# Kernel optimization log

Hardware: AMD Instinct MI355X
Metric: run time of the kernel (lower is better)

## Reference

```python
import jax, jax.numpy as jnp
import numpy as np

N_MET = 100_000
N_RXN = 50_000
E_SUB = 2_000_000
E_ALL = 4_000_000
MSG_DIM = 16
HIDDEN = 32


def setup_inputs() -> dict:
    key = jax.random.key(0)
    ks = jax.random.split(key, 16)
    x_met = jax.random.normal(ks[0], (N_MET,), dtype=jnp.float32)
    sto_sub = jax.random.uniform(ks[1], (E_SUB,), dtype=jnp.float32, minval=0.0, maxval=1.0)
    sto_all = jax.random.normal(ks[2], (E_ALL,), dtype=jnp.float32)
    met_sub = jax.random.randint(ks[3], (E_SUB,), 0, N_MET)
    rxn_sub = jax.random.randint(ks[4], (E_SUB,), 0, N_RXN)
    met_all = jax.random.randint(ks[5], (E_ALL,), 0, N_MET)
    rxn_all = jax.random.randint(ks[6], (E_ALL,), 0, N_RXN)
    # msg_mlp: Linear(2->HIDDEN), Tanh, Linear(HIDDEN->MSG_DIM)
    W1m = jax.random.normal(ks[7], (2, HIDDEN), jnp.float32) / np.sqrt(2.0)
    b1m = jnp.zeros((HIDDEN,), jnp.float32)
    W2m = jax.random.normal(ks[8], (HIDDEN, MSG_DIM), jnp.float32) / np.sqrt(HIDDEN)
    b2m = jnp.zeros((MSG_DIM,), jnp.float32)
    # rate_mlp: Linear(MSG_DIM->HIDDEN), Tanh, Linear(HIDDEN->1)
    W1r = jax.random.normal(ks[9], (MSG_DIM, HIDDEN), jnp.float32) / np.sqrt(MSG_DIM)
    b1r = jnp.zeros((HIDDEN,), jnp.float32)
    W2r = jax.random.normal(ks[10], (HIDDEN, 1), jnp.float32) / np.sqrt(HIDDEN)
    b2r = jnp.zeros((1,), jnp.float32)
    return {
        "x_met": x_met, "sto_sub": sto_sub, "sto_all": sto_all,
        "W1m": W1m, "b1m": b1m, "W2m": W2m, "b2m": b2m,
        "W1r": W1r, "b1r": b1r, "W2r": W2r, "b2r": b2r,
        "met_sub": met_sub, "rxn_sub": rxn_sub,
        "met_all": met_all, "rxn_all": rxn_all,
    }


def reference(x_met, sto_sub, sto_all, W1m, b1m, W2m, b2m, W1r, b1r, W2r, b2r,
              met_sub, rxn_sub, met_all, rxn_all):
    # gather substrate node features and build per-edge MLP input [E_sub, 2]
    msg_in = jnp.stack([x_met[met_sub], sto_sub], axis=-1)
    # msg MLP: tanh hidden, linear out -> [E_sub, MSG_DIM]
    msg = jnp.tanh(msg_in @ W1m + b1m) @ W2m + b2m
    # scatter-add messages into reactions -> [N_RXN, MSG_DIM]
    h_rxn = jax.ops.segment_sum(msg, rxn_sub, num_segments=N_RXN)
    # rate MLP + softplus -> per-reaction rate v [N_RXN]
    v = jax.nn.softplus((jnp.tanh(h_rxn @ W1r + b1r) @ W2r + b2r)[:, 0])
    # stoichiometric contributions scattered into metabolites -> dxdt [N_MET]
    contrib = sto_all * v[rxn_all]
    dxdt = jax.ops.segment_sum(contrib, met_all, num_segments=N_MET)
    return dxdt, v
```

## Files before the change

### kernel.cpp

```cpp
#include <hip/hip_runtime.h>

#define N_MET 100000
#define N_RXN 50000
#define E_SUB 2000000
#define E_ALL 4000000
#define MSG_DIM 16
#define HIDDEN 32

#define NBKT_A 391
#define NB_ALL 245
#define TILE_A 16384
#define LOFFA_W (NBKT_A + 1)
#define NBKT_S 782
#define NB_SUB 245
#define TILE_S 8192
#define SLOT_S 4096


__device__ __forceinline__ float fast_tanh(float x) {
    const float e = __expf(2.0f * x);
    return 1.0f - 2.0f * __builtin_amdgcn_rcpf(e + 1.0f);
}

__global__ __launch_bounds__(1024) void zero_gcnt_kernel(int* __restrict__ g)
{
    const int t = threadIdx.x;
    if (t < NBKT_S) g[t] = 0;
}


__global__ __launch_bounds__(1024) void scatter_bin_sub_kernel(
    const float* __restrict__ x_met, const float* __restrict__ sto_sub,
    const int* __restrict__ met_sub, const int* __restrict__ rxn_sub,
    int* __restrict__ gcnt, float2* __restrict__ pxs)
{
    __shared__ float2 se[TILE_S];
    __shared__ int cnt[NBKT_S];
    __shared__ int loff[NBKT_S + 1];
    __shared__ int roff[NBKT_S];
    const int t = threadIdx.x, bk = blockIdx.x;
    for (int i = t; i < NBKT_S; i += 1024) cnt[i] = 0;
    __syncthreads();

    const int e0 = bk * TILE_S;
    const int rem = min(TILE_S, E_SUB - e0);
    const int tb = 8 * t;
    float2 pay[8]; int meta[8];
    if (tb + 8 <= rem) {
        const int4 r01 = ((const int4*)(rxn_sub + e0))[2 * t];
        const int4 r23 = ((const int4*)(rxn_sub + e0))[2 * t + 1];
        const int4 m01 = ((const int4*)(met_sub + e0))[2 * t];
        const int4 m23 = ((const int4*)(met_sub + e0))[2 * t + 1];
        const float4 s01 = ((const float4*)(sto_sub + e0))[2 * t];
        const float4 s23 = ((const float4*)(sto_sub + e0))[2 * t + 1];
        const int rr[8] = {r01.x, r01.y, r01.z, r01.w, r23.x, r23.y, r23.z, r23.w};
        const int mm[8] = {m01.x, m01.y, m01.z, m01.w, m23.x, m23.y, m23.z, m23.w};
        const float ss[8] = {s01.x, s01.y, s01.z, s01.w, s23.x, s23.y, s23.z, s23.w};
#pragma unroll
        for (int k = 0; k < 8; ++k) {
            const int r = rr[k];
            const float x = x_met[mm[k]];
            const int sb = (__float_as_int(ss[k]) & ~63) | (r & 63);
            pay[k] = make_float2(x, __int_as_float(sb));
            const int q = r >> 6;
            meta[k] = (atomicAdd(&cnt[q], 1) << 10) | q;
        }
    } else {
#pragma unroll
        for (int k = 0; k < 8; ++k) {
            const int e = e0 + tb + k;
            if (e < E_SUB) {
                const int r = rxn_sub[e];
                const float x = x_met[met_sub[e]];
                const int sb = (__float_as_int(sto_sub[e]) & ~63) | (r & 63);
                pay[k] = make_float2(x, __int_as_float(sb));
                const int q = r >> 6;
                meta[k] = (atomicAdd(&cnt[q], 1) << 10) | q;
            } else meta[k] = -1;
        }
    }
    __syncthreads();

    if (t < 64) {
        int carry = 0;
        for (int bb = 0; bb < NBKT_S; bb += 64) {
            const int idx = bb + t;
            const int val = (idx < NBKT_S) ? cnt[idx] : 0;
            int x = val;
#pragma unroll
            for (int off = 1; off < 64; off <<= 1) {
                const int y = __shfl_up(x, off);
                if (t >= off) x += y;
            }
            if (idx < NBKT_S) loff[idx] = carry + x - val;
            carry += __shfl(x, 63);
        }
        if (t == 0) loff[NBKT_S] = carry;
    }
    __syncthreads();

#pragma unroll
    for (int k = 0; k < 8; ++k) {
        if (meta[k] >= 0)
            se[loff[meta[k] & 1023] + (meta[k] >> 10)] = pay[k];
    }
    for (int q = t; q < NBKT_S; q += 1024) {
        const int len = loff[q + 1] - loff[q];
        roff[q] = len ? atomicAdd(&gcnt[q], len) : 0;
    }
    __syncthreads();

    const int qw = t >> 4, ql = t & 15;
    for (int q = qw; q < NBKT_S; q += 64) {
        const int s = loff[q], len = loff[q + 1] - s;
        float2* d = pxs + (size_t)q * SLOT_S + roff[q];
        for (int i = ql; i < len; i += 16)
            d[i] = se[s + i];
    }
}

__global__ __launch_bounds__(512, 6) void bucket_msg_kernel(
    const float2* __restrict__ pxs, const int* __restrict__ gcnt,
    const float* __restrict__ W1m, const float* __restrict__ b1m,
    const float* __restrict__ W2m, const float* __restrict__ b2m,
    const float* __restrict__ W1r, const float* __restrict__ b1r,
    const float* __restrict__ W2r, const float* __restrict__ b2r,
    float* __restrict__ v)
{
    __shared__ float2 se[4096];
    __shared__ float  sth[64 * 33];
    __shared__ int    cnt[64];
    __shared__ int    soff[65];
    __shared__ int    ccnt[64];
    __shared__ float  sW2m[HIDDEN * MSG_DIM];
    __shared__ float  sb2m[MSG_DIM];
    __shared__ float  sW1r[MSG_DIM * HIDDEN];
    __shared__ float  sb1r[HIDDEN];
    __shared__ float  sW2r[HIDDEN];
    __shared__ float  sb2r;
    __shared__ float  sh[64 * 17];

    const int t = threadIdx.x;
    const int w = t >> 6, l = t & 63;
    const int half = l >> 5, j = l & 31;

    for (int i = t; i < HIDDEN * MSG_DIM; i += 512) sW2m[i] = W2m[i];
    for (int i = t; i < MSG_DIM * HIDDEN; i += 512) sW1r[i] = W1r[i];
    if (t < MSG_DIM) sb2m[t] = b2m[t];
    if (t < HIDDEN) sb1r[t] = b1r[t];
    if (t >= 64 && t < 64 + HIDDEN) sW2r[t - 64] = W2r[t - 64];
    if (t == 128) sb2r = b2r[0];
    if (t < 64) ccnt[t] = 0;

    const float w1x = W1m[j];
    const float w1y = W1m[HIDDEN + j];
    const float w1b = b1m[j];

    const int b = blockIdx.x;
    const int beg = b * SLOT_S;
    const int end = beg + gcnt[b];

    float acc[4] = {0.0f, 0.0f, 0.0f, 0.0f};

    for (int cb = beg; cb < end; cb += 4096) {
        if (t < 64) cnt[t] = 0;
        __syncthreads();

        float2 pay[8];
        int meta[8];
#pragma unroll
        for (int k = 0; k < 8; ++k) {
            const int idx = cb + t + (k << 9);
            if (idx < end) {
                const float2 pv = pxs[idx];
                const int r = __float_as_int(pv.y) & 63;
                meta[k] = (atomicAdd(&cnt[r], 1) << 6) | r;
                pay[k] = pv;
            } else meta[k] = -1;
        }
        __syncthreads();

        if (t < 64) {
            const int orig = cnt[t];
            int x = orig;
#pragma unroll
            for (int off = 1; off < 64; off <<= 1) {
                const int y = __shfl_up(x, off);
                if (t >= off) x += y;
            }
            soff[t] = x - orig;
            if (t == 63) soff[64] = x;
            ccnt[t] += orig;
        }
        __syncthreads();

#pragma unroll
        for (int k = 0; k < 8; ++k) {
            if (meta[k] >= 0)
                se[soff[meta[k] & 63] + (meta[k] >> 6)] = pay[k];
        }
        __syncthreads();

#pragma unroll
        for (int p = 0; p < 4; ++p) {
            const int q = (w << 3) + (p << 1) + half;
            const int rb = soff[q];
            const int rl = soff[q + 1] - rb;
            float a0 = 0.0f, a1 = 0.0f;
            int i = 0;
            for (; i + 2 <= rl; i += 2) {
                const float2 e0 = se[rb + i];
                const float2 e1 = se[rb + i + 1];
                a0 += fast_tanh(fmaf(e0.x, w1x, fmaf(e0.y, w1y, w1b)));
                a1 += fast_tanh(fmaf(e1.x, w1x, fmaf(e1.y, w1y, w1b)));
            }
            if (i < rl) {
                const float2 e0 = se[rb + i];
                a0 += fast_tanh(fmaf(e0.x, w1x, fmaf(e0.y, w1y, w1b)));
            }
            acc[p] += a0 + a1;
        }
        __syncthreads();
    }

#pragma unroll
    for (int p = 0; p < 4; ++p) {
        const int q = (w << 3) + (p << 1) + half;
        sth[q * 33 + j] = acc[p];
    }
    __syncthreads();

    {
        const int r = t & 63, g = (t >> 6) << 1;
        const float cntf = (float)ccnt[r];
        float h0 = cntf * sb2m[g + 0], h1 = cntf * sb2m[g + 1];
#pragma unroll 8
        for (int jj = 0; jj < HIDDEN; ++jj) {
            const float ts = sth[r * 33 + jj];
            h0 = fmaf(ts, sW2m[jj * MSG_DIM + g + 0], h0);
            h1 = fmaf(ts, sW2m[jj * MSG_DIM + g + 1], h1);
        }
        sh[r * 17 + g + 0] = h0;
        sh[r * 17 + g + 1] = h1;
    }
    __syncthreads();

    if (t < 64) {
        const int r = b * 64 + t;
        if (r < N_RXN) {
            float h[MSG_DIM];
#pragma unroll
            for (int d = 0; d < MSG_DIM; ++d) h[d] = sh[t * 17 + d];
            float acc2 = sb2r;
#pragma unroll 2
            for (int jj = 0; jj < HIDDEN; ++jj) {
                float z = sb1r[jj];
#pragma unroll
                for (int d = 0; d < MSG_DIM; ++d)
                    z = fmaf(h[d], sW1r[d * HIDDEN + jj], z);
                acc2 = fmaf(fast_tanh(z), sW2r[jj], acc2);
            }
            v[r] = fmaxf(acc2, 0.0f) + log1pf(expf(-fabsf(acc2)));
        }
    }
}


__global__ __launch_bounds__(1024) void scatter_bin_kernel(
    const float* __restrict__ sto_all, const float* __restrict__ v,
    const int* __restrict__ met_all, const int* __restrict__ rxn_all,
    int* __restrict__ loffA, float* __restrict__ pc)
{
    __shared__ float sp[TILE_A];
    __shared__ int cnt[NBKT_A];
    __shared__ int loff[NBKT_A + 1];
    const int t = threadIdx.x, bk = blockIdx.x;
    for (int i = t; i < NBKT_A; i += 1024) cnt[i] = 0;
    __syncthreads();

    const int e0 = bk * TILE_A;
    const int rem = min(TILE_A, E_ALL - e0);
    const int tb = 16 * t;
    int meta[16];
    const bool full = (tb + 16 <= rem);
    if (full) {
#pragma unroll
        for (int kk = 0; kk < 4; ++kk) {
            const int4 m = ((const int4*)(met_all + e0))[4 * t + kk];
            meta[4 * kk + 0] = (atomicAdd(&cnt[m.x >> 8], 1) << 17) | m.x;
            meta[4 * kk + 1] = (atomicAdd(&cnt[m.y >> 8], 1) << 17) | m.y;
            meta[4 * kk + 2] = (atomicAdd(&cnt[m.z >> 8], 1) << 17) | m.z;
            meta[4 * kk + 3] = (atomicAdd(&cnt[m.w >> 8], 1) << 17) | m.w;
        }
    } else {
#pragma unroll
        for (int k = 0; k < 16; ++k) {
            const int e = e0 + tb + k;
            if (e < E_ALL) {
                const int m = met_all[e];
                meta[k] = (atomicAdd(&cnt[m >> 8], 1) << 17) | m;
            } else meta[k] = -1;
        }
    }
    __syncthreads();

    if (t < 64) {
        int carry = 0;
        for (int bb = 0; bb < NBKT_A; bb += 64) {
            const int idx = bb + t;
            const int val = (idx < NBKT_A) ? cnt[idx] : 0;
            int x = val;
#pragma unroll
            for (int off = 1; off < 64; off <<= 1) {
                const int y = __shfl_up(x, off);
                if (t >= off) x += y;
            }
            if (idx < NBKT_A) loff[idx] = carry + x - val;
            carry += __shfl(x, 63);
        }
        if (t == 0) loff[NBKT_A] = carry;
    }
    __syncthreads();

    if (t < LOFFA_W) loffA[bk * LOFFA_W + t] = loff[t];

    if (full) {
#pragma unroll
        for (int kk = 0; kk < 4; ++kk) {
            const int4 r = ((const int4*)(rxn_all + e0))[4 * t + kk];
            const float4 s = ((const float4*)(sto_all + e0))[4 * t + kk];
            const int rr[4] = {r.x, r.y, r.z, r.w};
            const float ss[4] = {s.x, s.y, s.z, s.w};
#pragma unroll
            for (int u = 0; u < 4; ++u) {
                const int mt = meta[4 * kk + u];
                const int m = mt & 0x1FFFF;
                const float c = ss[u] * v[rr[u]];
                const int cb = (__float_as_int(c) & ~255) | (m & 255);
                sp[loff[m >> 8] + (mt >> 17)] = __int_as_float(cb);
            }
        }
    } else {
#pragma unroll
        for (int k = 0; k < 16; ++k) {
            const int e = e0 + tb + k;
            if (e < E_ALL) {
                const int mt = meta[k];
                const int m = mt & 0x1FFFF;
                const float c = sto_all[e] * v[rxn_all[e]];
                const int cb = (__float_as_int(c) & ~255) | (m & 255);
                sp[loff[m >> 8] + (mt >> 17)] = __int_as_float(cb);
            }
        }
    }
    __syncthreads();

    for (int i = 4 * t; i < rem; i += 4096)
        *(float4*)(pc + e0 + i) = *(const float4*)(sp + i);
}

__global__ __launch_bounds__(512) void bucket_accum_kernel(
    const float* __restrict__ pc, const int* __restrict__ loffA,
    float* __restrict__ dxdt)
{
    __shared__ float acc[256];
    const int q = blockIdx.x, t = threadIdx.x;
    const int w = t >> 6, lane = t & 63;
    if (t < 256) acc[t] = 0.0f;
    __syncthreads();

    const int nt = (NB_ALL - 1 - w) / 8 + 1;
    int sv = 0, ev = 0;
    if (lane < nt) {
        const int tile = w + 8 * lane;
        sv = loffA[tile * LOFFA_W + q];
        ev = loffA[tile * LOFFA_W + q + 1];
    }
    for (int it = 0; it < nt; ++it) {
        const int s = __shfl(sv, it);
        const int e = __shfl(ev, it);
        const int tbase = (w + 8 * it) * TILE_A;
        for (int i = s + lane; i < e; i += 64) {
            const float pv = pc[tbase + i];
            atomicAdd(&acc[__float_as_int(pv) & 255], pv);
        }
    }
    __syncthreads();
    if (t < 256) {
        const int met = q * 256 + t;
        if (met < N_MET) dxdt[met] = acc[t];
    }
}

extern "C" void kernel_launch(void* const* d_in, const int* in_sizes, int n_in,
                              void* d_out, int out_size, void* d_ws, size_t ws_size,
                              hipStream_t stream) {
    const float* x_met   = (const float*)d_in[0];
    const float* sto_sub = (const float*)d_in[1];
    const float* sto_all = (const float*)d_in[2];
    const float* W1m     = (const float*)d_in[3];
    const float* b1m     = (const float*)d_in[4];
    const float* W2m     = (const float*)d_in[5];
    const float* b2m     = (const float*)d_in[6];
    const float* W1r     = (const float*)d_in[7];
    const float* b1r     = (const float*)d_in[8];
    const float* W2r     = (const float*)d_in[9];
    const float* b2r     = (const float*)d_in[10];
    const int*   met_sub = (const int*)d_in[11];
    const int*   rxn_sub = (const int*)d_in[12];
    const int*   met_all = (const int*)d_in[13];
    const int*   rxn_all = (const int*)d_in[14];

    float* dxdt = (float*)d_out;
    float* v    = dxdt + N_MET;

    char* ws = (char*)d_ws;
    int* gcnt   = (int*)ws;  ws += ((sizeof(int) * NBKT_S + 15) / 16) * 16;
    int* loffA  = (int*)ws;  ws += (((size_t)NB_ALL * LOFFA_W * 4 + 15) / 16) * 16;
    char* P = ws;
    float2* pxs = (float2*)P;
    float*  pc  = (float*)P;

    zero_gcnt_kernel<<<1, 1024, 0, stream>>>(gcnt);
    scatter_bin_sub_kernel<<<NB_SUB, 1024, 0, stream>>>(
        x_met, sto_sub, met_sub, rxn_sub, gcnt, pxs);
    bucket_msg_kernel<<<NBKT_S, 512, 0, stream>>>(
        pxs, gcnt, W1m, b1m, W2m, b2m, W1r, b1r, W2r, b2r, v);

    scatter_bin_kernel<<<NB_ALL, 1024, 0, stream>>>(
        sto_all, v, met_all, rxn_all, loffA, pc);
    bucket_accum_kernel<<<NBKT_A, 512, 0, stream>>>(pc, loffA, dxdt);
}
```

Before: 234.0 us.

## Scatter binned contributions into per-bucket global slots via atomic offsets

The all-edge scatter kernel now reserves space in a fixed-size global slot per metabolite bucket with an atomicAdd on a global counter. It copies each bucket's run from shared memory into that slot, instead of writing the whole tile back in tile order. The accumulate kernel then streams one contiguous slot per bucket with float4 loads, replacing the walk over 245 per-tile segments. The cost is a non-coalesced, 16-lane-per-bucket copy-out in the scatter kernel, global atomics, and a fixed slot capacity of 12288 per bucket that relies on the uniform index distribution.

```diff
diff --git a/kernel.cpp b/kernel.cpp
--- a/kernel.cpp
+++ b/kernel.cpp
@@ -10,7 +10,7 @@
 #define NBKT_A 391
 #define NB_ALL 245
 #define TILE_A 16384
-#define LOFFA_W (NBKT_A + 1)
+#define SLOT_A 12288
 #define NBKT_S 782
 #define NB_SUB 245
 #define TILE_S 8192
@@ -22,10 +22,12 @@
     return 1.0f - 2.0f * __builtin_amdgcn_rcpf(e + 1.0f);
 }
 
-__global__ __launch_bounds__(1024) void zero_gcnt_kernel(int* __restrict__ g)
+__global__ __launch_bounds__(1024) void zero_cnt_kernel(
+    int* __restrict__ gs, int* __restrict__ ga)
 {
     const int t = threadIdx.x;
-    if (t < NBKT_S) g[t] = 0;
+    for (int i = t; i < NBKT_S; i += 1024) gs[i] = 0;
+    for (int i = t; i < NBKT_A; i += 1024) ga[i] = 0;
 }
 
 
@@ -269,11 +271,12 @@
 __global__ __launch_bounds__(1024) void scatter_bin_kernel(
     const float* __restrict__ sto_all, const float* __restrict__ v,
     const int* __restrict__ met_all, const int* __restrict__ rxn_all,
-    int* __restrict__ loffA, float* __restrict__ pc)
+    int* __restrict__ gcntA, float* __restrict__ pc)
 {
     __shared__ float sp[TILE_A];
     __shared__ int cnt[NBKT_A];
     __shared__ int loff[NBKT_A + 1];
+    __shared__ int roff[NBKT_A];
     const int t = threadIdx.x, bk = blockIdx.x;
     for (int i = t; i < NBKT_A; i += 1024) cnt[i] = 0;
     __syncthreads();
@@ -322,7 +325,10 @@
     }
     __syncthreads();
 
-    if (t < LOFFA_W) loffA[bk * LOFFA_W + t] = loff[t];
+    for (int q = t; q < NBKT_A; q += 1024) {
+        const int len = loff[q + 1] - loff[q];
+        roff[q] = len ? atomicAdd(&gcntA[q], len) : 0;
+    }
 
     if (full) {
 #pragma unroll
@@ -355,35 +361,36 @@
     }
     __syncthreads();
 
-    for (int i = 4 * t; i < rem; i += 4096)
-        *(float4*)(pc + e0 + i) = *(const float4*)(sp + i);
+    const int qw = t >> 4, ql = t & 15;
+    for (int q = qw; q < NBKT_A; q += 64) {
+        const int s = loff[q], len = loff[q + 1] - s;
+        float* d = pc + (size_t)q * SLOT_A + roff[q];
+        for (int i = ql; i < len; i += 16)
+            d[i] = sp[s + i];
+    }
 }
 
 __global__ __launch_bounds__(512) void bucket_accum_kernel(
-    const float* __restrict__ pc, const int* __restrict__ loffA,
+    const float* __restrict__ pc, const int* __restrict__ gcntA,
     float* __restrict__ dxdt)
 {
     __shared__ float acc[256];
     const int q = blockIdx.x, t = threadIdx.x;
-    const int w = t >> 6, lane = t & 63;
     if (t < 256) acc[t] = 0.0f;
     __syncthreads();
-
-    const int nt = (NB_ALL - 1 - w) / 8 + 1;
-    int sv = 0, ev = 0;
-    if (lane < nt) {
-        const int tile = w + 8 * lane;
-        sv = loffA[tile * LOFFA_W + q];
-        ev = loffA[tile * LOFFA_W + q + 1];
-    }
-    for (int it = 0; it < nt; ++it) {
-        const int s = __shfl(sv, it);
-        const int e = __shfl(ev, it);
-        const int tbase = (w + 8 * it) * TILE_A;
-        for (int i = s + lane; i < e; i += 64) {
-            const float pv = pc[tbase + i];
-            atomicAdd(&acc[__float_as_int(pv) & 255], pv);
-        }
+    const float* s = pc + (size_t)q * SLOT_A;
+    const int n = gcntA[q];
+    const int n4 = n & ~3;
+    for (int i = 4 * t; i < n4; i += 2048) {
+        const float4 pv = *(const float4*)(s + i);
+        atomicAdd(&acc[__float_as_int(pv.x) & 255], pv.x);
+        atomicAdd(&acc[__float_as_int(pv.y) & 255], pv.y);
+        atomicAdd(&acc[__float_as_int(pv.z) & 255], pv.z);
+        atomicAdd(&acc[__float_as_int(pv.w) & 255], pv.w);
+    }
+    for (int i = n4 + t; i < n; i += 512) {
+        const float pv = s[i];
+        atomicAdd(&acc[__float_as_int(pv) & 255], pv);
     }
     __syncthreads();
     if (t < 256) {
@@ -415,19 +422,20 @@
     float* v    = dxdt + N_MET;
 
     char* ws = (char*)d_ws;
-    int* gcnt   = (int*)ws;  ws += ((sizeof(int) * NBKT_S + 15) / 16) * 16;
-    int* loffA  = (int*)ws;  ws += (((size_t)NB_ALL * LOFFA_W * 4 + 15) / 16) * 16;
+    int* gcntS  = (int*)ws;  ws += ((sizeof(int) * NBKT_S + 15) / 16) * 16;
+    int* gcntA  = (int*)ws;  ws += ((sizeof(int) * NBKT_A + 15) / 16) * 16;
     char* P = ws;
     float2* pxs = (float2*)P;
     float*  pc  = (float*)P;
 
-    zero_gcnt_kernel<<<1, 1024, 0, stream>>>(gcnt);
+    zero_cnt_kernel<<<1, 1024, 0, stream>>>(gcntS, gcntA);
+
     scatter_bin_sub_kernel<<<NB_SUB, 1024, 0, stream>>>(
-        x_met, sto_sub, met_sub, rxn_sub, gcnt, pxs);
+        x_met, sto_sub, met_sub, rxn_sub, gcntS, pxs);
     bucket_msg_kernel<<<NBKT_S, 512, 0, stream>>>(
-        pxs, gcnt, W1m, b1m, W2m, b2m, W1r, b1r, W2r, b2r, v);
+        pxs, gcntS, W1m, b1m, W2m, b2m, W1r, b1r, W2r, b2r, v);
 
     scatter_bin_kernel<<<NB_ALL, 1024, 0, stream>>>(
-        sto_all, v, met_all, rxn_all, loffA, pc);
-    bucket_accum_kernel<<<NBKT_A, 512, 0, stream>>>(pc, loffA, dxdt);
-}
+        sto_all, v, met_all, rxn_all, gcntA, pc);
+    bucket_accum_kernel<<<NBKT_A, 512, 0, stream>>>(pc, gcntA, dxdt);
+}
```

Measured after the change: 235.6 us. Within noise of the previous version (+0.7%).
